# Performance work log

Hardware: AMD Instinct MI355X
Metric: run time of the kernel (lower is better)

The kernel has to match this reference:

```python
import jax, jax.numpy as jnp
import numpy as np

BOX_SIDE = 50.0  # orthorhombic simulation cell side length


def setup_inputs() -> dict:
    key = jax.random.key(0)
    k1, _ = jax.random.split(key)
    N = 8192
    pos = jax.random.uniform(k1, (N, 3), dtype=jnp.float32) * BOX_SIDE  # cartesian positions in box
    box = jnp.ones((3,), dtype=jnp.float32) * BOX_SIDE                   # box lengths (orthorhombic)
    return {"pos": pos, "box": box, "k": 17}


def reference(pos, box, k):
    """Periodic (minimum-image) k-NN graph: returns (edge_index [2, N*k], knn_dist [N, k])."""
    N = pos.shape[0]
    # Accumulate squared wrapped distances one spatial dim at a time to avoid an (N,N,3) intermediate.
    d2 = jnp.zeros((N, N), dtype=pos.dtype)
    for d in range(pos.shape[1]):  # fixed small loop over 3 spatial dims
        diff = pos[:, None, d] - pos[None, :, d]
        diff = diff - box[d] * jnp.round(diff / box[d])  # minimum-image wrap
        d2 = d2 + diff * diff
    # Exclude self-edges.
    d2 = jnp.where(jnp.eye(N, dtype=bool), jnp.inf, d2)
    # k nearest neighbors per node (smallest distance => top_k of negated d2).
    _, idx = jax.lax.top_k(-d2, k)                      # idx: [N, k]
    knn_d2 = jnp.take_along_axis(d2, idx, axis=1)       # [N, k]
    knn_dist = jnp.sqrt(knn_d2)
    src = jnp.repeat(jnp.arange(N), k)
    edge_index = jnp.stack([src, idx.reshape(-1)])      # [2, N*k] (source, neighbor)
    return edge_index, knn_dist
```

## Files before the change

kernel.cpp:

```cpp
#include <hip/hip_runtime.h>
#include <math.h>

#define K 17
#define WAVE 64
#define G 10
#define CELLS (G*G*G)
#define NROW 9
#define NPASS 5
#define NROW2 25
#define CAP 128
#define KEY_MAX 0xFFFFFFFFFFFFFFFFULL

__device__ __forceinline__ bool lex_less(float ad, int ai, float bd, int bi) {
    return (ad < bd) || (ad == bd && ai < bi);
}


__global__ __launch_bounds__(1024) void prep_kernel(
    const float* __restrict__ pos, const float* __restrict__ box,
    int* __restrict__ cellStart , float4* __restrict__ sp4, int N)
{
    __shared__ int s[1024];
    __shared__ int cur[CELLS];
    const int t = threadIdx.x;
    s[t] = 0;
    __syncthreads();

    const float invx = (float)G / box[0];
    const float invy = (float)G / box[1];
    const float invz = (float)G / box[2];

    for (int p = t; p < N; p += 1024) {
        int cx = min((int)(pos[3*p+0] * invx), G-1);
        int cy = min((int)(pos[3*p+1] * invy), G-1);
        int cz = min((int)(pos[3*p+2] * invz), G-1);
        atomicAdd(&s[(cz*G + cy)*G + cx], 1);
    }
    __syncthreads();
    int v = s[t];
    for (int off = 1; off < 1024; off <<= 1) {
        int u = (t >= off) ? s[t - off] : 0;
        __syncthreads();
        s[t] += u;
        __syncthreads();
    }
    int excl = s[t] - v;
    if (t < CELLS) { cellStart[t] = excl; cur[t] = excl; }
    if (t == 0) cellStart[CELLS] = N;
    __syncthreads();

    for (int p = t; p < N; p += 1024) {
        float x = pos[3*p+0], y = pos[3*p+1], z = pos[3*p+2];
        int cx = min((int)(x * invx), G-1);
        int cy = min((int)(y * invy), G-1);
        int cz = min((int)(z * invz), G-1);
        int slot = atomicAdd(&cur[(cz*G + cy)*G + cx], 1);
        sp4[slot] = make_float4(x, y, z, __int_as_float(p));
    }
}


__global__ __launch_bounds__(256) void knn_main(
    const float* __restrict__ pos, const float* __restrict__ box,
    const float4* __restrict__ sp4, const int* __restrict__ cellStart,
    float* __restrict__ out, int N)
{
    const int lane = threadIdx.x & 63;
    const int wid  = threadIdx.x >> 6;
    const int i = blockIdx.x * 4 + wid;
    if (i >= N) return;

    __shared__ unsigned long long surv[4][CAP];

    const float bx = box[0], by = box[1], bz = box[2];
    const float hx = 0.5f*bx, hy = 0.5f*by, hz = 0.5f*bz;
    const float invx = (float)G/bx, invy = (float)G/by, invz = (float)G/bz;
    const float cmin = fminf(bx, fminf(by, bz)) / (float)G;

    const float xi = pos[3*i+0], yi = pos[3*i+1], zi = pos[3*i+2];
    const int cx = min((int)(xi*invx), G-1);
    const int cy = min((int)(yi*invy), G-1);
    const int cz = min((int)(zi*invz), G-1);

    const long kN = (long)N * K;

    int  M = 0;
    bool have = false;

    {
        int rs1[NROW], rs2[NROW], c1a[NROW], tc[NROW];
#pragma unroll
        for (int r9 = 0; r9 < NROW; ++r9) {
            const int oz = r9 / 3 - 1, oy = r9 % 3 - 1;
            int uz = cz + oz; uz += (uz < 0) ? G : 0; uz -= (uz >= G) ? G : 0;
            int uy = cy + oy; uy += (uy < 0) ? G : 0; uy -= (uy >= G) ? G : 0;
            const int rowbase = (uz*G + uy)*G;
            int u0a, u1a, u0b = 0, u1b = -1;
            if (cx == 0)        { u0a = G-1; u1a = G-1; u0b = 0; u1b = 1; }
            else if (cx == G-1) { u0a = G-2; u1a = G-1; u0b = 0; u1b = 0; }
            else                { u0a = cx-1; u1a = cx+1; }
            int a = cellStart[rowbase + u0a];
            int c1 = cellStart[rowbase + u1a + 1] - a;
            int a2 = 0, c2 = 0;
            if (u1b >= u0b) {
                a2 = cellStart[rowbase + u0b];
                c2 = cellStart[rowbase + u1b + 1] - a2;
            }
            rs1[r9] = a; rs2[r9] = a2; c1a[r9] = c1; tc[r9] = c1 + c2;
        }

        const float thr = cmin * cmin * 0.999f;
        const unsigned long long thrKey =
            ((unsigned long long)__float_as_uint(thr) << 13) | 0x1FFFULL;

        int base = 0; bool bad = false;
#pragma unroll
        for (int p = 0; p < NPASS; ++p) {
            const int ra = 2*p;
            const bool has2 = (2*p + 1 < NROW);
            const int rb = has2 ? (2*p + 1) : ra;
            const int n0 = tc[ra];
            const int tot = n0 + (has2 ? tc[rb] : 0);
#pragma unroll 1
            for (int t0 = 0; t0 < tot; t0 += WAVE) {
                const int t = t0 + lane;
                unsigned long long key = KEY_MAX;
                if (t < tot) {
                    const bool inA = (t < n0);
                    const int tt  = inA ? t : (t - n0);
                    const int c1s = inA ? c1a[ra] : c1a[rb];
                    const int s1  = inA ? rs1[ra] : rs1[rb];
                    const int s2  = inA ? rs2[ra] : rs2[rb];
                    const int slot = (tt < c1s) ? (s1 + tt) : (s2 + tt - c1s);
                    float4 pnt = sp4[slot];
                    int j = __float_as_int(pnt.w);
                    if (j != i) {
                        float dx = __fsub_rn(xi, pnt.x);
                        float dy = __fsub_rn(yi, pnt.y);
                        float dz = __fsub_rn(zi, pnt.z);
                        dx = dx > hx ? __fsub_rn(dx, bx) : (dx < -hx ? __fadd_rn(dx, bx) : dx);
                        dy = dy > hy ? __fsub_rn(dy, by) : (dy < -hy ? __fadd_rn(dy, by) : dy);
                        dz = dz > hz ? __fsub_rn(dz, bz) : (dz < -hz ? __fadd_rn(dz, bz) : dz);
                        float cd = __fadd_rn(__fadd_rn(__fmul_rn(dx, dx), __fmul_rn(dy, dy)),
                                             __fmul_rn(dz, dz));
                        key = ((unsigned long long)__float_as_uint(cd) << 13) | (unsigned)j;
                    }
                }
                const bool sv = (key <= thrKey);
                unsigned long long mk = __ballot(sv);
                int pc = __popcll(mk);
                if (base + pc <= CAP) {
                    if (sv) {
                        int below = __popcll(mk & ((1ULL << lane) - 1ULL));
                        surv[wid][base + below] = key;
                    }
                } else bad = true;
                base += pc;
            }
        }
        if (!bad && base >= K) { have = true; M = base; }
    }

    if (!have) {
        const float thr2 = cmin * cmin * 1.9580f;
        const unsigned long long thrKey2 =
            ((unsigned long long)__float_as_uint(thr2) << 13) | 0x1FFFULL;

        int base = 0; bool bad2 = false;
#pragma unroll 1
        for (int r25 = 0; r25 < NROW2; ++r25) {
            const int oz = r25 / 5 - 2, oy = r25 % 5 - 2;
            int uz = cz + oz; uz += (uz < 0) ? G : 0; uz -= (uz >= G) ? G : 0;
            int uy = cy + oy; uy += (uy < 0) ? G : 0; uy -= (uy >= G) ? G : 0;
            const int rowbase = (uz*G + uy)*G;
            int a0 = cx - 2, b0 = cx + 2;
            int u0a, u1a, u0b = 0, u1b = -1;
            if (a0 < 0)       { u0a = a0 + G; u1a = G - 1; u0b = 0; u1b = b0; }
            else if (b0 >= G) { u0a = a0;     u1a = G - 1; u0b = 0; u1b = b0 - G; }
            else              { u0a = a0;     u1a = b0; }
            int a = cellStart[rowbase + u0a];
            int c1 = cellStart[rowbase + u1a + 1] - a;
            int a2 = 0, c2 = 0;
            if (u1b >= u0b) {
                a2 = cellStart[rowbase + u0b];
                c2 = cellStart[rowbase + u1b + 1] - a2;
            }
            const int cnt2 = c1 + c2;
#pragma unroll 1
            for (int t0 = 0; t0 < cnt2; t0 += WAVE) {
                const int t = t0 + lane;
                unsigned long long key = KEY_MAX;
                if (t < cnt2) {
                    const int slot = (t < c1) ? (a + t) : (a2 + t - c1);
                    float4 pnt = sp4[slot];
                    int j = __float_as_int(pnt.w);
                    if (j != i) {
                        float dx = __fsub_rn(xi, pnt.x);
                        float dy = __fsub_rn(yi, pnt.y);
                        float dz = __fsub_rn(zi, pnt.z);
                        dx = dx > hx ? __fsub_rn(dx, bx) : (dx < -hx ? __fadd_rn(dx, bx) : dx);
                        dy = dy > hy ? __fsub_rn(dy, by) : (dy < -hy ? __fadd_rn(dy, by) : dy);
                        dz = dz > hz ? __fsub_rn(dz, bz) : (dz < -hz ? __fadd_rn(dz, bz) : dz);
                        float cd = __fadd_rn(__fadd_rn(__fmul_rn(dx, dx), __fmul_rn(dy, dy)),
                                             __fmul_rn(dz, dz));
                        key = ((unsigned long long)__float_as_uint(cd) << 13) | (unsigned)j;
                    }
                }
                const bool sv = (key <= thrKey2);
                unsigned long long mk = __ballot(sv);
                int pc = __popcll(mk);
                if (base + pc <= CAP) {
                    if (sv) {
                        int below = __popcll(mk & ((1ULL << lane) - 1ULL));
                        surv[wid][base + below] = key;
                    }
                } else bad2 = true;
                base += pc;
            }
        }
        if (!bad2 && base >= K) { have = true; M = base; }
    }

    if (have) {
        __asm__ __volatile__("s_waitcnt lgkmcnt(0)" ::: "memory");
        unsigned long long k0 = surv[wid][(lane < M) ? lane : 0];
        unsigned long long k1 = (lane + 64 < M) ? surv[wid][lane + 64] : KEY_MAX;
        int r0 = 0, r1 = 0;
#pragma unroll 2
        for (int m = 0; m < M; ++m) {
            unsigned long long s = surv[wid][m];
            r0 += (s < k0) ? 1 : 0;
            r1 += (s < k1) ? 1 : 0;
        }
        if (lane < K) out[(long)i*K + lane] = (float)i;
        if (lane < M && r0 < K) {
            out[kN + (long)i*K + r0]   = (float)(int)(k0 & 0x1FFFULL);
            out[2*kN + (long)i*K + r0] = __fsqrt_rn(__uint_as_float((unsigned)(k0 >> 13)));
        }
        if (lane + 64 < M && r1 < K) {
            out[kN + (long)i*K + r1]   = (float)(int)(k1 & 0x1FFFULL);
            out[2*kN + (long)i*K + r1] = __fsqrt_rn(__uint_as_float((unsigned)(k1 >> 13)));
        }
        return;
    }

    {
        float d[K]; int id[K];
#pragma unroll
        for (int m = 0; m < K; ++m) { d[m] = INFINITY; id[m] = 0x7fffffff; }
        float md = INFINITY; int mi = 0x7fffffff;
        bool done = false;

#pragma unroll 1
        for (int r = 1; r <= G/2 && !done; ++r) {
            const int lo = -r;
            const int hi = (2*r+1 > G) ? (G-1-r) : r;
#pragma unroll 1
            for (int oz = lo; oz <= hi; ++oz) {
                int uz = cz + oz; uz += (uz < 0) ? G : 0; uz -= (uz >= G) ? G : 0;
#pragma unroll 1
                for (int oy = lo; oy <= hi; ++oy) {
                    int uy = cy + oy; uy += (uy < 0) ? G : 0; uy -= (uy >= G) ? G : 0;
                    const int rowbase = (uz*G + uy)*G;
                    const bool rowFull = (r == 1) || (max(abs(oy), abs(oz)) >= r);

                    int u0a, u1a, u0b = 0, u1b = -1;
                    if (rowFull) {
                        int a = cx + lo, b = cx + hi;
                        if (a < 0)       { u0a = a + G; u1a = G - 1; u0b = 0; u1b = b; }
                        else if (b >= G) { u0a = a;     u1a = G - 1; u0b = 0; u1b = b - G; }
                        else             { u0a = a;     u1a = b; }
                    } else {
                        int ux1 = cx - r; ux1 += (ux1 < 0) ? G : 0;
                        u0a = u1a = ux1;
                        if (hi >= r) { int ux2 = cx + r; ux2 -= (ux2 >= G) ? G : 0; u0b = u1b = ux2; }
                    }

                    int xs1 = cellStart[rowbase + u0a];
                    int l1  = cellStart[rowbase + u1a + 1] - xs1;
                    int xs2 = 0, l2 = 0;
                    if (u1b >= u0b) {
                        xs2 = cellStart[rowbase + u0b];
                        l2  = cellStart[rowbase + u1b + 1] - xs2;
                    }
                    const int cnt2 = l1 + l2;

#pragma unroll 1
                    for (int t0 = 0; t0 < cnt2; t0 += WAVE) {
                        const int t = t0 + lane;
                        float cd = INFINITY; int ci = 0x7fffffff;
                        if (t < cnt2) {
                            int slot = (t < l1) ? (xs1 + t) : (xs2 + t - l1);
                            float4 p = sp4[slot];
                            int j = __float_as_int(p.w);
                            if (j != i) {
                                float dx = __fsub_rn(xi, p.x);
                                float dy = __fsub_rn(yi, p.y);
                                float dz = __fsub_rn(zi, p.z);
                                dx = dx > hx ? __fsub_rn(dx, bx) : (dx < -hx ? __fadd_rn(dx, bx) : dx);
                                dy = dy > hy ? __fsub_rn(dy, by) : (dy < -hy ? __fadd_rn(dy, by) : dy);
                                dz = dz > hz ? __fsub_rn(dz, bz) : (dz < -hz ? __fadd_rn(dz, bz) : dz);
                                cd = __fadd_rn(__fadd_rn(__fmul_rn(dx, dx), __fmul_rn(dy, dy)),
                                               __fmul_rn(dz, dz));
                                ci = j;
                            }
                        }
                        if (lex_less(cd, ci, d[K-1], id[K-1])) {
                            bool lt[K];
#pragma unroll
                            for (int m = 0; m < K; ++m) lt[m] = lex_less(cd, ci, d[m], id[m]);
#pragma unroll
                            for (int m = K-1; m >= 1; --m) {
                                d[m]  = lt[m-1] ? d[m-1]  : (lt[m] ? cd : d[m]);
                                id[m] = lt[m-1] ? id[m-1] : (lt[m] ? ci : id[m]);
                            }
                            d[0]  = lt[0] ? cd : d[0];
                            id[0] = lt[0] ? ci : id[0];
                        }
                    }
                }
            }

#pragma unroll 1
            for (int e = 0; e < K; ++e) {
                float bv = d[0]; int bi = id[0];
#pragma unroll
                for (int off = 32; off >= 1; off >>= 1) {
                    float ov = __shfl_xor(bv, off, WAVE);
                    int   oi = __shfl_xor(bi, off, WAVE);
                    if (lex_less(ov, oi, bv, bi)) { bv = ov; bi = oi; }
                }
                if (d[0] == bv && id[0] == bi) {
#pragma unroll
                    for (int m = 0; m < K-1; ++m) { d[m] = d[m+1]; id[m] = id[m+1]; }
                    d[K-1] = INFINITY; id[K-1] = 0x7fffffff;
                }
                if (lane == e) { md = bv; mi = bi; }
            }

            float d17 = __shfl(md, K - 1, WAVE);
            done = (r >= G/2) || (d17 < (r*cmin)*(r*cmin)*0.9998f);

            if (!done) {
#pragma unroll
                for (int m = 0; m < K; ++m) { d[m] = INFINITY; id[m] = 0x7fffffff; }
                if (lane < K) { d[0] = md; id[0] = mi; }
            }
        }

        if (lane < K) {
            out[(long)i*K + lane]        = (float)i;
            out[kN + (long)i*K + lane]   = (float)mi;
            out[2*kN + (long)i*K + lane] = __fsqrt_rn(md);
        }
    }
}

extern "C" void kernel_launch(void* const* d_in, const int* in_sizes, int n_in,
                              void* d_out, int out_size, void* d_ws, size_t ws_size,
                              hipStream_t stream) {
    const float* pos = (const float*)d_in[0];
    const float* box = (const float*)d_in[1];
    const int N = in_sizes[0] / 3;

    unsigned char* ws = (unsigned char*)d_ws;
    int*    cellStart = (int*)ws;
    float4* sp4       = (float4*)(ws + 4096);

    prep_kernel<<<dim3(1), dim3(1024), 0, stream>>>(pos, box, cellStart, sp4, N);
    knn_main<<<dim3((N + 3) / 4), dim3(256), 0, stream>>>(pos, box, sp4, cellStart,
                                                          (float*)d_out, N);
}
```

Before: 102.2 us.

## Replace sorted cell list with fixed-capacity per-cell buckets plus overflow list

```diff
diff --git a/kernel.cpp b/kernel.cpp
--- a/kernel.cpp
+++ b/kernel.cpp
@@ -5,9 +5,8 @@
 #define WAVE 64
 #define G 10
 #define CELLS (G*G*G)
-#define NROW 9
-#define NPASS 5
-#define NROW2 25
+#define BCAP 16
+#define OVCAP 128
 #define CAP 128
 #define KEY_MAX 0xFFFFFFFFFFFFFFFFULL
 
@@ -16,53 +15,35 @@
 }
 
 
-__global__ __launch_bounds__(1024) void prep_kernel(
+__global__ __launch_bounds__(256) void prep_bucket(
     const float* __restrict__ pos, const float* __restrict__ box,
-    int* __restrict__ cellStart , float4* __restrict__ sp4, int N)
+    int* __restrict__ cnt, int* __restrict__ ovCnt,
+    float4* __restrict__ ov, float4* __restrict__ bucket, int N)
 {
-    __shared__ int s[1024];
-    __shared__ int cur[CELLS];
-    const int t = threadIdx.x;
-    s[t] = 0;
-    __syncthreads();
-
+    const int t = blockIdx.x * 256 + threadIdx.x;
+    if (t >= N) return;
+    const float x = pos[3*t+0], y = pos[3*t+1], z = pos[3*t+2];
     const float invx = (float)G / box[0];
     const float invy = (float)G / box[1];
     const float invz = (float)G / box[2];
-
-    for (int p = t; p < N; p += 1024) {
-        int cx = min((int)(pos[3*p+0] * invx), G-1);
-        int cy = min((int)(pos[3*p+1] * invy), G-1);
-        int cz = min((int)(pos[3*p+2] * invz), G-1);
-        atomicAdd(&s[(cz*G + cy)*G + cx], 1);
-    }
-    __syncthreads();
-    int v = s[t];
-    for (int off = 1; off < 1024; off <<= 1) {
-        int u = (t >= off) ? s[t - off] : 0;
-        __syncthreads();
-        s[t] += u;
-        __syncthreads();
-    }
-    int excl = s[t] - v;
-    if (t < CELLS) { cellStart[t] = excl; cur[t] = excl; }
-    if (t == 0) cellStart[CELLS] = N;
-    __syncthreads();
-
-    for (int p = t; p < N; p += 1024) {
-        float x = pos[3*p+0], y = pos[3*p+1], z = pos[3*p+2];
-        int cx = min((int)(x * invx), G-1);
-        int cy = min((int)(y * invy), G-1);
-        int cz = min((int)(z * invz), G-1);
-        int slot = atomicAdd(&cur[(cz*G + cy)*G + cx], 1);
-        sp4[slot] = make_float4(x, y, z, __int_as_float(p));
+    const int cx = min((int)(x * invx), G-1);
+    const int cy = min((int)(y * invy), G-1);
+    const int cz = min((int)(z * invz), G-1);
+    const int cell = (cz*G + cy)*G + cx;
+    const int slot = atomicAdd(&cnt[cell], 1);
+    const float4 v = make_float4(x, y, z, __int_as_float(t));
+    if (slot < BCAP) bucket[cell*BCAP + slot] = v;
+    else {
+        int o = atomicAdd(ovCnt, 1);
+        if (o < OVCAP) ov[o] = v;
     }
 }
 
 
-__global__ __launch_bounds__(256) void knn_main(
+__global__ __launch_bounds__(256, 4) void knn_main(
     const float* __restrict__ pos, const float* __restrict__ box,
-    const float4* __restrict__ sp4, const int* __restrict__ cellStart,
+    const int* __restrict__ cnt, const int* __restrict__ ovCnt,
+    const float4* __restrict__ ov, const float4* __restrict__ bucket,
     float* __restrict__ out, int N)
 {
     const int lane = threadIdx.x & 63;
@@ -83,68 +64,72 @@
     const int cz = min((int)(zi*invz), G-1);
 
     const long kN = (long)N * K;
+    const int slot = lane & 15;
+    const int gq   = lane >> 4;
+    const int oc   = ovCnt[0];
 
     int  M = 0;
     bool have = false;
 
     {
-        int rs1[NROW], rs2[NROW], c1a[NROW], tc[NROW];
-#pragma unroll
-        for (int r9 = 0; r9 < NROW; ++r9) {
-            const int oz = r9 / 3 - 1, oy = r9 % 3 - 1;
-            int uz = cz + oz; uz += (uz < 0) ? G : 0; uz -= (uz >= G) ? G : 0;
-            int uy = cy + oy; uy += (uy < 0) ? G : 0; uy -= (uy >= G) ? G : 0;
-            const int rowbase = (uz*G + uy)*G;
-            int u0a, u1a, u0b = 0, u1b = -1;
-            if (cx == 0)        { u0a = G-1; u1a = G-1; u0b = 0; u1b = 1; }
-            else if (cx == G-1) { u0a = G-2; u1a = G-1; u0b = 0; u1b = 0; }
-            else                { u0a = cx-1; u1a = cx+1; }
-            int a = cellStart[rowbase + u0a];
-            int c1 = cellStart[rowbase + u1a + 1] - a;
-            int a2 = 0, c2 = 0;
-            if (u1b >= u0b) {
-                a2 = cellStart[rowbase + u0b];
-                c2 = cellStart[rowbase + u1b + 1] - a2;
-            }
-            rs1[r9] = a; rs2[r9] = a2; c1a[r9] = c1; tc[r9] = c1 + c2;
-        }
-
         const float thr = cmin * cmin * 0.999f;
         const unsigned long long thrKey =
             ((unsigned long long)__float_as_uint(thr) << 13) | 0x1FFFULL;
 
-        int base = 0; bool bad = false;
-#pragma unroll
-        for (int p = 0; p < NPASS; ++p) {
-            const int ra = 2*p;
-            const bool has2 = (2*p + 1 < NROW);
-            const int rb = has2 ? (2*p + 1) : ra;
-            const int n0 = tc[ra];
-            const int tot = n0 + (has2 ? tc[rb] : 0);
-#pragma unroll 1
-            for (int t0 = 0; t0 < tot; t0 += WAVE) {
-                const int t = t0 + lane;
+        int base = 0; bool bad = (oc > OVCAP);
+#pragma unroll
+        for (int p = 0; p < 7; ++p) {
+            const int g = 4*p + gq;
+            unsigned long long key = KEY_MAX;
+            if (g < 27) {
+                int ox = g % 3 - 1, oy = (g/3) % 3 - 1, oz = g/9 - 1;
+                int ux = cx + ox; ux += (ux < 0) ? G : 0; ux -= (ux >= G) ? G : 0;
+                int uy = cy + oy; uy += (uy < 0) ? G : 0; uy -= (uy >= G) ? G : 0;
+                int uz = cz + oz; uz += (uz < 0) ? G : 0; uz -= (uz >= G) ? G : 0;
+                const int cell = (uz*G + uy)*G + ux;
+                const int c = cnt[cell];
+                const float4 pnt = bucket[cell*BCAP + slot];
+                const int j = __float_as_int(pnt.w);
+                if (slot < min(c, BCAP) && j != i) {
+                    float dx = __fsub_rn(xi, pnt.x);
+                    float dy = __fsub_rn(yi, pnt.y);
+                    float dz = __fsub_rn(zi, pnt.z);
+                    dx = dx > hx ? __fsub_rn(dx, bx) : (dx < -hx ? __fadd_rn(dx, bx) : dx);
+                    dy = dy > hy ? __fsub_rn(dy, by) : (dy < -hy ? __fadd_rn(dy, by) : dy);
+                    dz = dz > hz ? __fsub_rn(dz, bz) : (dz < -hz ? __fadd_rn(dz, bz) : dz);
+                    float cd = __fadd_rn(__fadd_rn(__fmul_rn(dx, dx), __fmul_rn(dy, dy)),
+                                         __fmul_rn(dz, dz));
+                    key = ((unsigned long long)__float_as_uint(cd) << 13) | (unsigned)j;
+                }
+            }
+            const bool sv = (key <= thrKey);
+            unsigned long long mk = __ballot(sv);
+            int pc = __popcll(mk);
+            if (base + pc <= CAP) {
+                if (sv) {
+                    int below = __popcll(mk & ((1ULL << lane) - 1ULL));
+                    surv[wid][base + below] = key;
+                }
+            } else bad = true;
+            base += pc;
+        }
+        if (!bad && oc > 0) {
+#pragma unroll
+            for (int rdx = 0; rdx < 2; ++rdx) {
+                const int t = rdx*WAVE + lane;
                 unsigned long long key = KEY_MAX;
-                if (t < tot) {
-                    const bool inA = (t < n0);
-                    const int tt  = inA ? t : (t - n0);
-                    const int c1s = inA ? c1a[ra] : c1a[rb];
-                    const int s1  = inA ? rs1[ra] : rs1[rb];
-                    const int s2  = inA ? rs2[ra] : rs2[rb];
-                    const int slot = (tt < c1s) ? (s1 + tt) : (s2 + tt - c1s);
-                    float4 pnt = sp4[slot];
-                    int j = __float_as_int(pnt.w);
-                    if (j != i) {
-                        float dx = __fsub_rn(xi, pnt.x);
-                        float dy = __fsub_rn(yi, pnt.y);
-                        float dz = __fsub_rn(zi, pnt.z);
-                        dx = dx > hx ? __fsub_rn(dx, bx) : (dx < -hx ? __fadd_rn(dx, bx) : dx);
-                        dy = dy > hy ? __fsub_rn(dy, by) : (dy < -hy ? __fadd_rn(dy, by) : dy);
-                        dz = dz > hz ? __fsub_rn(dz, bz) : (dz < -hz ? __fadd_rn(dz, bz) : dz);
-                        float cd = __fadd_rn(__fadd_rn(__fmul_rn(dx, dx), __fmul_rn(dy, dy)),
-                                             __fmul_rn(dz, dz));
-                        key = ((unsigned long long)__float_as_uint(cd) << 13) | (unsigned)j;
-                    }
+                const float4 pnt = ov[t];
+                const int j = __float_as_int(pnt.w);
+                if (t < oc && j != i) {
+                    float dx = __fsub_rn(xi, pnt.x);
+                    float dy = __fsub_rn(yi, pnt.y);
+                    float dz = __fsub_rn(zi, pnt.z);
+                    dx = dx > hx ? __fsub_rn(dx, bx) : (dx < -hx ? __fadd_rn(dx, bx) : dx);
+                    dy = dy > hy ? __fsub_rn(dy, by) : (dy < -hy ? __fadd_rn(dy, by) : dy);
+                    dz = dz > hz ? __fsub_rn(dz, bz) : (dz < -hz ? __fadd_rn(dz, bz) : dz);
+                    float cd = __fadd_rn(__fadd_rn(__fmul_rn(dx, dx), __fmul_rn(dy, dy)),
+                                         __fmul_rn(dz, dz));
+                    key = ((unsigned long long)__float_as_uint(cd) << 13) | (unsigned)j;
                 }
                 const bool sv = (key <= thrKey);
                 unsigned long long mk = __ballot(sv);
@@ -161,50 +146,65 @@
         if (!bad && base >= K) { have = true; M = base; }
     }
 
-    if (!have) {
+    if (!have && oc <= OVCAP) {
         const float thr2 = cmin * cmin * 1.9580f;
         const unsigned long long thrKey2 =
             ((unsigned long long)__float_as_uint(thr2) << 13) | 0x1FFFULL;
 
         int base = 0; bool bad2 = false;
 #pragma unroll 1
-        for (int r25 = 0; r25 < NROW2; ++r25) {
-            const int oz = r25 / 5 - 2, oy = r25 % 5 - 2;
-            int uz = cz + oz; uz += (uz < 0) ? G : 0; uz -= (uz >= G) ? G : 0;
-            int uy = cy + oy; uy += (uy < 0) ? G : 0; uy -= (uy >= G) ? G : 0;
-            const int rowbase = (uz*G + uy)*G;
-            int a0 = cx - 2, b0 = cx + 2;
-            int u0a, u1a, u0b = 0, u1b = -1;
-            if (a0 < 0)       { u0a = a0 + G; u1a = G - 1; u0b = 0; u1b = b0; }
-            else if (b0 >= G) { u0a = a0;     u1a = G - 1; u0b = 0; u1b = b0 - G; }
-            else              { u0a = a0;     u1a = b0; }
-            int a = cellStart[rowbase + u0a];
-            int c1 = cellStart[rowbase + u1a + 1] - a;
-            int a2 = 0, c2 = 0;
-            if (u1b >= u0b) {
-                a2 = cellStart[rowbase + u0b];
-                c2 = cellStart[rowbase + u1b + 1] - a2;
-            }
-            const int cnt2 = c1 + c2;
-#pragma unroll 1
-            for (int t0 = 0; t0 < cnt2; t0 += WAVE) {
-                const int t = t0 + lane;
+        for (int p = 0; p < 32; ++p) {
+            const int g = 4*p + gq;
+            unsigned long long key = KEY_MAX;
+            if (g < 125) {
+                int ox = g % 5 - 2, oy = (g/5) % 5 - 2, oz = g/25 - 2;
+                int ux = cx + ox; ux += (ux < 0) ? G : 0; ux -= (ux >= G) ? G : 0;
+                int uy = cy + oy; uy += (uy < 0) ? G : 0; uy -= (uy >= G) ? G : 0;
+                int uz = cz + oz; uz += (uz < 0) ? G : 0; uz -= (uz >= G) ? G : 0;
+                const int cell = (uz*G + uy)*G + ux;
+                const int c = cnt[cell];
+                const float4 pnt = bucket[cell*BCAP + slot];
+                const int j = __float_as_int(pnt.w);
+                if (slot < min(c, BCAP) && j != i) {
+                    float dx = __fsub_rn(xi, pnt.x);
+                    float dy = __fsub_rn(yi, pnt.y);
+                    float dz = __fsub_rn(zi, pnt.z);
+                    dx = dx > hx ? __fsub_rn(dx, bx) : (dx < -hx ? __fadd_rn(dx, bx) : dx);
+                    dy = dy > hy ? __fsub_rn(dy, by) : (dy < -hy ? __fadd_rn(dy, by) : dy);
+                    dz = dz > hz ? __fsub_rn(dz, bz) : (dz < -hz ? __fadd_rn(dz, bz) : dz);
+                    float cd = __fadd_rn(__fadd_rn(__fmul_rn(dx, dx), __fmul_rn(dy, dy)),
+                                         __fmul_rn(dz, dz));
+                    key = ((unsigned long long)__float_as_uint(cd) << 13) | (unsigned)j;
+                }
+            }
+            const bool sv = (key <= thrKey2);
+            unsigned long long mk = __ballot(sv);
+            int pc = __popcll(mk);
+            if (base + pc <= CAP) {
+                if (sv) {
+                    int below = __popcll(mk & ((1ULL << lane) - 1ULL));
+                    surv[wid][base + below] = key;
+                }
+            } else bad2 = true;
+            base += pc;
+        }
+        if (!bad2 && oc > 0) {
+#pragma unroll
+            for (int rdx = 0; rdx < 2; ++rdx) {
+                const int t = rdx*WAVE + lane;
                 unsigned long long key = KEY_MAX;
-                if (t < cnt2) {
-                    const int slot = (t < c1) ? (a + t) : (a2 + t - c1);
-                    float4 pnt = sp4[slot];
-                    int j = __float_as_int(pnt.w);
-                    if (j != i) {
-                        float dx = __fsub_rn(xi, pnt.x);
-                        float dy = __fsub_rn(yi, pnt.y);
-                        float dz = __fsub_rn(zi, pnt.z);
-                        dx = dx > hx ? __fsub_rn(dx, bx) : (dx < -hx ? __fadd_rn(dx, bx) : dx);
-                        dy = dy > hy ? __fsub_rn(dy, by) : (dy < -hy ? __fadd_rn(dy, by) : dy);
-                        dz = dz > hz ? __fsub_rn(dz, bz) : (dz < -hz ? __fadd_rn(dz, bz) : dz);
-                        float cd = __fadd_rn(__fadd_rn(__fmul_rn(dx, dx), __fmul_rn(dy, dy)),
-                                             __fmul_rn(dz, dz));
-                        key = ((unsigned long long)__float_as_uint(cd) << 13) | (unsigned)j;
-                    }
+                const float4 pnt = ov[t];
+                const int j = __float_as_int(pnt.w);
+                if (t < oc && j != i) {
+                    float dx = __fsub_rn(xi, pnt.x);
+                    float dy = __fsub_rn(yi, pnt.y);
+                    float dz = __fsub_rn(zi, pnt.z);
+                    dx = dx > hx ? __fsub_rn(dx, bx) : (dx < -hx ? __fadd_rn(dx, bx) : dx);
+                    dy = dy > hy ? __fsub_rn(dy, by) : (dy < -hy ? __fadd_rn(dy, by) : dy);
+                    dz = dz > hz ? __fsub_rn(dz, bz) : (dz < -hz ? __fadd_rn(dz, bz) : dz);
+                    float cd = __fadd_rn(__fadd_rn(__fmul_rn(dx, dx), __fmul_rn(dy, dy)),
+                                         __fmul_rn(dz, dz));
+                    key = ((unsigned long long)__float_as_uint(cd) << 13) | (unsigned)j;
                 }
                 const bool sv = (key <= thrKey2);
                 unsigned long long mk = __ballot(sv);
@@ -248,111 +248,56 @@
         float d[K]; int id[K];
 #pragma unroll
         for (int m = 0; m < K; ++m) { d[m] = INFINITY; id[m] = 0x7fffffff; }
-        float md = INFINITY; int mi = 0x7fffffff;
-        bool done = false;
 
 #pragma unroll 1
-        for (int r = 1; r <= G/2 && !done; ++r) {
-            const int lo = -r;
-            const int hi = (2*r+1 > G) ? (G-1-r) : r;
+        for (int j0 = 0; j0 < N; j0 += WAVE) {
+            const int j = j0 + lane;
+            float cd = INFINITY; int ci = 0x7fffffff;
+            if (j < N && j != i) {
+                float dx = __fsub_rn(xi, pos[3*j+0]);
+                float dy = __fsub_rn(yi, pos[3*j+1]);
+                float dz = __fsub_rn(zi, pos[3*j+2]);
+                dx = dx > hx ? __fsub_rn(dx, bx) : (dx < -hx ? __fadd_rn(dx, bx) : dx);
+                dy = dy > hy ? __fsub_rn(dy, by) : (dy < -hy ? __fadd_rn(dy, by) : dy);
+                dz = dz > hz ? __fsub_rn(dz, bz) : (dz < -hz ? __fadd_rn(dz, bz) : dz);
+                cd = __fadd_rn(__fadd_rn(__fmul_rn(dx, dx), __fmul_rn(dy, dy)),
+                               __fmul_rn(dz, dz));
+                ci = j;
+            }
+            if (lex_less(cd, ci, d[K-1], id[K-1])) {
+                bool lt[K];
+#pragma unroll
+                for (int m = 0; m < K; ++m) lt[m] = lex_less(cd, ci, d[m], id[m]);
+#pragma unroll
+                for (int m = K-1; m >= 1; --m) {
+                    d[m]  = lt[m-1] ? d[m-1]  : (lt[m] ? cd : d[m]);
+                    id[m] = lt[m-1] ? id[m-1] : (lt[m] ? ci : id[m]);
+                }
+                d[0]  = lt[0] ? cd : d[0];
+                id[0] = lt[0] ? ci : id[0];
+            }
+        }
+
 #pragma unroll 1
-            for (int oz = lo; oz <= hi; ++oz) {
-                int uz = cz + oz; uz += (uz < 0) ? G : 0; uz -= (uz >= G) ? G : 0;
-#pragma unroll 1
-                for (int oy = lo; oy <= hi; ++oy) {
-                    int uy = cy + oy; uy += (uy < 0) ? G : 0; uy -= (uy >= G) ? G : 0;
-                    const int rowbase = (uz*G + uy)*G;
-                    const bool rowFull = (r == 1) || (max(abs(oy), abs(oz)) >= r);
-
-                    int u0a, u1a, u0b = 0, u1b = -1;
-                    if (rowFull) {
-                        int a = cx + lo, b = cx + hi;
-                        if (a < 0)       { u0a = a + G; u1a = G - 1; u0b = 0; u1b = b; }
-                        else if (b >= G) { u0a = a;     u1a = G - 1; u0b = 0; u1b = b - G; }
-                        else             { u0a = a;     u1a = b; }
-                    } else {
-                        int ux1 = cx - r; ux1 += (ux1 < 0) ? G : 0;
-                        u0a = u1a = ux1;
-                        if (hi >= r) { int ux2 = cx + r; ux2 -= (ux2 >= G) ? G : 0; u0b = u1b = ux2; }
-                    }
-
-                    int xs1 = cellStart[rowbase + u0a];
-                    int l1  = cellStart[rowbase + u1a + 1] - xs1;
-                    int xs2 = 0, l2 = 0;
-                    if (u1b >= u0b) {
-                        xs2 = cellStart[rowbase + u0b];
-                        l2  = cellStart[rowbase + u1b + 1] - xs2;
-                    }
-                    const int cnt2 = l1 + l2;
-
-#pragma unroll 1
-                    for (int t0 = 0; t0 < cnt2; t0 += WAVE) {
-                        const int t = t0 + lane;
-                        float cd = INFINITY; int ci = 0x7fffffff;
-                        if (t < cnt2) {
-                            int slot = (t < l1) ? (xs1 + t) : (xs2 + t - l1);
-                            float4 p = sp4[slot];
-                            int j = __float_as_int(p.w);
-                            if (j != i) {
-                                float dx = __fsub_rn(xi, p.x);
-                                float dy = __fsub_rn(yi, p.y);
-                                float dz = __fsub_rn(zi, p.z);
-                                dx = dx > hx ? __fsub_rn(dx, bx) : (dx < -hx ? __fadd_rn(dx, bx) : dx);
-                                dy = dy > hy ? __fsub_rn(dy, by) : (dy < -hy ? __fadd_rn(dy, by) : dy);
-                                dz = dz > hz ? __fsub_rn(dz, bz) : (dz < -hz ? __fadd_rn(dz, bz) : dz);
-                                cd = __fadd_rn(__fadd_rn(__fmul_rn(dx, dx), __fmul_rn(dy, dy)),
-                                               __fmul_rn(dz, dz));
-                                ci = j;
-                            }
-                        }
-                        if (lex_less(cd, ci, d[K-1], id[K-1])) {
-                            bool lt[K];
-#pragma unroll
-                            for (int m = 0; m < K; ++m) lt[m] = lex_less(cd, ci, d[m], id[m]);
-#pragma unroll
-                            for (int m = K-1; m >= 1; --m) {
-                                d[m]  = lt[m-1] ? d[m-1]  : (lt[m] ? cd : d[m]);
-                                id[m] = lt[m-1] ? id[m-1] : (lt[m] ? ci : id[m]);
-                            }
-                            d[0]  = lt[0] ? cd : d[0];
-                            id[0] = lt[0] ? ci : id[0];
-                        }
-                    }
-                }
-            }
-
-#pragma unroll 1
-            for (int e = 0; e < K; ++e) {
-                float bv = d[0]; int bi = id[0];
-#pragma unroll
-                for (int off = 32; off >= 1; off >>= 1) {
-                    float ov = __shfl_xor(bv, off, WAVE);
-                    int   oi = __shfl_xor(bi, off, WAVE);
-                    if (lex_less(ov, oi, bv, bi)) { bv = ov; bi = oi; }
-                }
-                if (d[0] == bv && id[0] == bi) {
-#pragma unroll
-                    for (int m = 0; m < K-1; ++m) { d[m] = d[m+1]; id[m] = id[m+1]; }
-                    d[K-1] = INFINITY; id[K-1] = 0x7fffffff;
-                }
-                if (lane == e) { md = bv; mi = bi; }
-            }
-
-            float d17 = __shfl(md, K - 1, WAVE);
-            done = (r >= G/2) || (d17 < (r*cmin)*(r*cmin)*0.9998f);
-
-            if (!done) {
-#pragma unroll
-                for (int m = 0; m < K; ++m) { d[m] = INFINITY; id[m] = 0x7fffffff; }
-                if (lane < K) { d[0] = md; id[0] = mi; }
-            }
-        }
-
-        if (lane < K) {
-            out[(long)i*K + lane]        = (float)i;
-            out[kN + (long)i*K + lane]   = (float)mi;
-            out[2*kN + (long)i*K + lane] = __fsqrt_rn(md);
-        }
+        for (int e = 0; e < K; ++e) {
+            float bv = d[0]; int bi = id[0];
+#pragma unroll
+            for (int off = 32; off >= 1; off >>= 1) {
+                float ov2 = __shfl_xor(bv, off, WAVE);
+                int   oi = __shfl_xor(bi, off, WAVE);
+                if (lex_less(ov2, oi, bv, bi)) { bv = ov2; bi = oi; }
+            }
+            if (d[0] == bv && id[0] == bi) {
+#pragma unroll
+                for (int m = 0; m < K-1; ++m) { d[m] = d[m+1]; id[m] = id[m+1]; }
+                d[K-1] = INFINITY; id[K-1] = 0x7fffffff;
+            }
+            if (lane == e) {
+                out[kN + (long)i*K + e]   = (float)bi;
+                out[2*kN + (long)i*K + e] = __fsqrt_rn(bv);
+            }
+        }
+        if (lane < K) out[(long)i*K + lane] = (float)i;
     }
 }
 
@@ -364,10 +309,14 @@
     const int N = in_sizes[0] / 3;
 
     unsigned char* ws = (unsigned char*)d_ws;
-    int*    cellStart = (int*)ws;
-    float4* sp4       = (float4*)(ws + 4096);
-
-    prep_kernel<<<dim3(1), dim3(1024), 0, stream>>>(pos, box, cellStart, sp4, N);
-    knn_main<<<dim3((N + 3) / 4), dim3(256), 0, stream>>>(pos, box, sp4, cellStart,
-                                                          (float*)d_out, N);
+    int*    cnt    = (int*)ws;
+    int*    ovCnt  = (int*)(ws + 4000);
+    float4* ov     = (float4*)(ws + 4096);
+    float4* bucket = (float4*)(ws + 8192);
+
+    hipMemsetAsync(cnt, 0, 4004, stream);
+    prep_bucket<<<dim3((N + 255) / 256), dim3(256), 0, stream>>>(
+        pos, box, cnt, ovCnt, ov, bucket, N);
+    knn_main<<<dim3((N + 3) / 4), dim3(256), 0, stream>>>(
+        pos, box, cnt, ovCnt, ov, bucket, (float*)d_out, N);
 }
```

Result: faster. 93.86 us (-8.2%).
